# Kernel tuning notes

Hardware: AMD Instinct MI355X
Metric: run time of the kernel (lower is better)

The kernel has to match this reference:

```python
import jax, jax.numpy as jnp
import numpy as np

N, IN_C, OUT_C, E = 10000, 256, 64, 640000


def setup_inputs() -> dict:
    key = jax.random.key(0)
    ks = jax.random.split(key, 12)
    f32 = jnp.float32
    inp = {
        "x": jax.random.normal(ks[0], (N, N), f32),
        "edge_index": jax.random.randint(ks[1], (2, E), 0, N, jnp.int32),
        # trans: Linear(node_num -> in_channels)
        "Wt": jax.random.normal(ks[2], (N, IN_C), f32) / np.float32(np.sqrt(N)),
        "bt": jnp.zeros((IN_C,), f32),
        # conv1: ChebConv(IN_C -> 2*OUT_C), K=2 -> two weight matrices
        "W0_1": jax.random.normal(ks[3], (IN_C, 2 * OUT_C), f32) / np.float32(np.sqrt(IN_C)),
        "W1_1": jax.random.normal(ks[4], (IN_C, 2 * OUT_C), f32) / np.float32(np.sqrt(IN_C)),
        "b1": jnp.zeros((2 * OUT_C,), f32),
        # conv_mu / conv_logstd: ChebConv(2*OUT_C -> OUT_C), K=2
        "W0_mu": jax.random.normal(ks[5], (2 * OUT_C, OUT_C), f32) / np.float32(np.sqrt(2 * OUT_C)),
        "W1_mu": jax.random.normal(ks[6], (2 * OUT_C, OUT_C), f32) / np.float32(np.sqrt(2 * OUT_C)),
        "b_mu": jnp.zeros((OUT_C,), f32),
        "W0_ls": jax.random.normal(ks[7], (2 * OUT_C, OUT_C), f32) / np.float32(np.sqrt(2 * OUT_C)),
        "W1_ls": jax.random.normal(ks[8], (2 * OUT_C, OUT_C), f32) / np.float32(np.sqrt(2 * OUT_C)),
        "b_ls": jnp.zeros((OUT_C,), f32),
    }
    return inp


def _edge_norm(edge_index, n, dtype):
    """ChebConv K=2, sym norm, lambda_max=2: scaled Laplacian L_hat = -D^{-1/2} A D^{-1/2}.
    Returns per-edge weight w_e = -dinv[src] * dinv[dst]."""
    src, dst = edge_index[0], edge_index[1]
    deg = jax.ops.segment_sum(jnp.ones(src.shape, dtype), src, num_segments=n)
    dinv = jnp.where(deg > 0, jax.lax.rsqrt(jnp.maximum(deg, 1.0)), 0.0)
    return -dinv[src] * dinv[dst]


def _cheb(x, src, dst, w, W0, W1, b):
    # Tx_0 = x ; Tx_1 = L_hat @ x via gather-scale-scatter (K=2 stops here)
    tx1 = jax.ops.segment_sum(w[:, None] * x[src], dst, num_segments=x.shape[0])
    return x @ W0 + tx1 @ W1 + b


def reference(x, edge_index, Wt, bt, W0_1, W1_1, b1,
              W0_mu, W1_mu, b_mu, W0_ls, W1_ls, b_ls):
    n = x.shape[0]
    src, dst = edge_index[0], edge_index[1]
    w = _edge_norm(edge_index, n, x.dtype)  # shared across the three convs
    h = jax.nn.relu(x @ Wt + bt)                              # [N, IN_C]
    h = jax.nn.relu(_cheb(h, src, dst, w, W0_1, W1_1, b1))     # [N, 2*OUT_C]
    mu = _cheb(h, src, dst, w, W0_mu, W1_mu, b_mu)             # [N, OUT_C]
    logstd = _cheb(h, src, dst, w, W0_ls, W1_ls, b_ls)         # [N, OUT_C]
    return (mu, logstd)
```

## Files before the change

### kernel.cpp

```cpp
#include <hip/hip_runtime.h>

typedef unsigned short ushort_t;
typedef __bf16 bf16x8 __attribute__((ext_vector_type(8)));
typedef float f32x4 __attribute__((ext_vector_type(4)));

#define GN 10000
#define GE 640000
#define INC 256
#define HID 128
#define OUTC 64

constexpr size_t OFF_WTT   = 0;
constexpr size_t OFF_P     = 5120000;
constexpr size_t OFF_H     = 46276608;
constexpr size_t OFF_TX1   = 56516608;
constexpr size_t OFF_H2    = 66756608;
constexpr size_t OFF_TX2   = 71876608;
constexpr size_t OFF_DEG   = 76996608;
constexpr size_t OFF_INDEG = 77037568;
constexpr size_t OFF_CUR   = 77078528;
constexpr size_t OFF_RP    = 77119488;
constexpr size_t OFF_DINV  = 77160448;
constexpr size_t OFF_CSRC  = 77201408;
constexpr size_t OFF_CSW   = 79761408;

__device__ __forceinline__ ushort_t f2bf(float f) {
  unsigned int u = __float_as_uint(f);
  u += 0x7fffu + ((u >> 16) & 1u);
  return (ushort_t)(u >> 16);
}

__global__ __launch_bounds__(256) void zero_ints(int* __restrict__ p) {
  p[blockIdx.x * 256 + threadIdx.x] = 0;
}

__global__ __launch_bounds__(256) void transpose_wt(const float* __restrict__ Wt,
                                                    ushort_t* __restrict__ WtT) {
  __shared__ float tile[32][33];
  const int tx = threadIdx.x & 31, ty = threadIdx.x >> 5;
  const int k0 = blockIdx.x * 32, c0 = blockIdx.y * 32;
#pragma unroll
  for (int j = 0; j < 4; ++j) {
    const int k = k0 + ty + j * 8;
    if (k < GN) tile[ty + j * 8][tx] = Wt[(size_t)k * INC + c0 + tx];
  }
  __syncthreads();
#pragma unroll
  for (int j = 0; j < 4; ++j) {
    const int c = c0 + ty + j * 8;
    const int k = k0 + tx;
    if (k < GN) WtT[(size_t)c * GN + k] = f2bf(tile[tx][ty + j * 8]);
  }
}

__global__ __launch_bounds__(256) void count_deg(const int* __restrict__ src,
                                                 const int* __restrict__ dst,
                                                 int* __restrict__ outdeg,
                                                 int* __restrict__ indeg) {
  const int e = blockIdx.x * 256 + threadIdx.x;
  atomicAdd(&outdeg[src[e]], 1);
  atomicAdd(&indeg[dst[e]], 1);
}

__global__ __launch_bounds__(256) void dinv_kernel(const int* __restrict__ outdeg,
                                                   float* __restrict__ dinv) {
  const int i = blockIdx.x * 256 + threadIdx.x;
  if (i < GN) {
    const int d = outdeg[i];
    dinv[i] = (d > 0) ? rsqrtf((float)d) : 0.f;
  }
}

__global__ __launch_bounds__(1024) void scan_kernel(const int* __restrict__ indeg,
                                                    int* __restrict__ row_ptr) {
  __shared__ int sdata[1024];
  const int t = threadIdx.x;
  const int base = t * 10;
  int loc[10];
  int s = 0;
#pragma unroll
  for (int j = 0; j < 10; ++j) {
    const int idx = base + j;
    const int v = (idx < GN) ? indeg[idx] : 0;
    loc[j] = v;
    s += v;
  }
  sdata[t] = s;
  __syncthreads();
  for (int off = 1; off < 1024; off <<= 1) {
    int v = 0;
    if (t >= off) v = sdata[t - off];
    __syncthreads();
    if (t >= off) sdata[t] += v;
    __syncthreads();
  }
  int run = sdata[t] - s;
#pragma unroll
  for (int j = 0; j < 10; ++j) {
    const int idx = base + j;
    if (idx <= GN) row_ptr[idx] = run;
    if (idx < GN) run += loc[j];
  }
}

__global__ __launch_bounds__(256) void fill_csr(const int* __restrict__ src,
                                                const int* __restrict__ dst,
                                                const float* __restrict__ dinv,
                                                const int* __restrict__ row_ptr,
                                                int* __restrict__ cursor,
                                                int* __restrict__ csr_src,
                                                float* __restrict__ csr_w) {
  const int e = blockIdx.x * 256 + threadIdx.x;
  const int s = src[e];
  const int d = dst[e];
  const float w = -dinv[s] * dinv[d];
  const int pos = atomicAdd(&cursor[d], 1);
  const int slot = row_ptr[d] + pos;
  csr_src[slot] = s;
  csr_w[slot] = w;
}

__global__ __launch_bounds__(256) void gemm1_kernel(const float* __restrict__ x,
                                                    const ushort_t* __restrict__ WtT,
                                                    float* __restrict__ P) {
  constexpr int LDK = 72;
  __shared__ __align__(16) ushort_t As[64 * LDK];
  __shared__ __align__(16) ushort_t Bs[256 * LDK];
  const int t = threadIdx.x;
  const int rowbase = blockIdx.x * 64;
  const int ks = blockIdx.y;
  const int kbeg = ks * 2560;
  const int kend = min(kbeg + 2560, GN);
  const int nit = (kend - kbeg + 63) >> 6;
  const int lane = t & 63, wave = t >> 6;
  const int m16 = lane & 15, quad = lane >> 4;

  f32x4 acc[4][4];
#pragma unroll
  for (int i = 0; i < 4; ++i)
#pragma unroll
    for (int j = 0; j < 4; ++j) acc[i][j] = {0.f, 0.f, 0.f, 0.f};

  const int ar = t >> 4;
  const int ak = (t & 15) << 2;
  const int bn = t >> 3;
  const int bk = (t & 7) << 3;

  for (int it = 0; it < nit; ++it) {
    const int k0 = kbeg + (it << 6);
#pragma unroll
    for (int i = 0; i < 4; ++i) {
      const int r = ar + i * 16;
      const int row = rowbase + r;
      const int gk = k0 + ak;
      float4 v = make_float4(0.f, 0.f, 0.f, 0.f);
      if (row < GN && gk < kend) v = *(const float4*)(x + (size_t)row * GN + gk);
      ushort4 o = make_ushort4(f2bf(v.x), f2bf(v.y), f2bf(v.z), f2bf(v.w));
      *reinterpret_cast<ushort4*>(&As[r * LDK + ak]) = o;
    }
#pragma unroll
    for (int i = 0; i < 8; ++i) {
      const int n = bn + i * 32;
      const int gk = k0 + bk;
      uint4 v = make_uint4(0u, 0u, 0u, 0u);
      if (gk < kend) v = *(const uint4*)(WtT + (size_t)n * GN + gk);
      *reinterpret_cast<uint4*>(&Bs[n * LDK + bk]) = v;
    }
    __syncthreads();
#pragma unroll
    for (int hh = 0; hh < 2; ++hh) {
      const int kk = hh * 32 + quad * 8;
      bf16x8 a[4], b[4];
#pragma unroll
      for (int mi = 0; mi < 4; ++mi)
        a[mi] = *reinterpret_cast<const bf16x8*>(&As[(mi * 16 + m16) * LDK + kk]);
#pragma unroll
      for (int ni = 0; ni < 4; ++ni)
        b[ni] = *reinterpret_cast<const bf16x8*>(&Bs[(wave * 64 + ni * 16 + m16) * LDK + kk]);
#pragma unroll
      for (int mi = 0; mi < 4; ++mi)
#pragma unroll
        for (int ni = 0; ni < 4; ++ni)
          acc[mi][ni] = __builtin_amdgcn_mfma_f32_16x16x32_bf16(a[mi], b[ni], acc[mi][ni], 0, 0, 0);
    }
    __syncthreads();
  }
#pragma unroll
  for (int mi = 0; mi < 4; ++mi)
#pragma unroll
    for (int ni = 0; ni < 4; ++ni) {
      const int col = wave * 64 + ni * 16 + m16;
      const int row0 = rowbase + mi * 16 + quad * 4;
      float* p = P + ((size_t)ks * 10048 + row0) * 256 + col;
#pragma unroll
      for (int r = 0; r < 4; ++r) p[(size_t)r * 256] = acc[mi][ni][r];
    }
}

__global__ __launch_bounds__(256) void combine_kernel(const float* __restrict__ P,
                                                      const float* __restrict__ bt,
                                                      float* __restrict__ h) {
  const int tid = blockIdx.x * 256 + threadIdx.x;
  const int i = tid >> 6;
  const int c = (tid & 63) << 2;
  const size_t stride = (size_t)10048 * 256;
  const size_t base = (size_t)i * 256 + c;
  const float4 p0 = *(const float4*)(P + 0 * stride + base);
  const float4 p1 = *(const float4*)(P + 1 * stride + base);
  const float4 p2 = *(const float4*)(P + 2 * stride + base);
  const float4 p3 = *(const float4*)(P + 3 * stride + base);
  const float4 bv = *(const float4*)(bt + c);
  float4 o;
  o.x = fmaxf(p0.x + p1.x + p2.x + p3.x + bv.x, 0.f);
  o.y = fmaxf(p0.y + p1.y + p2.y + p3.y + bv.y, 0.f);
  o.z = fmaxf(p0.z + p1.z + p2.z + p3.z + bv.z, 0.f);
  o.w = fmaxf(p0.w + p1.w + p2.w + p3.w + bv.w, 0.f);
  *(float4*)(h + base) = o;
}

template <int C, int NPB>
__global__ __launch_bounds__(256) void spmm_kernel(const float* __restrict__ h,
                                                   const int* __restrict__ row_ptr,
                                                   const int* __restrict__ csr_src,
                                                   const float* __restrict__ csr_w,
                                                   float* __restrict__ tx) {
  const int d = blockIdx.x * NPB + (int)(threadIdx.x / C);
  const int c = threadIdx.x % C;
  const int beg = row_ptr[d];
  const int end = row_ptr[d + 1];
  float acc = 0.f;
#pragma unroll 4
  for (int j = beg; j < end; ++j) {
    const int s = csr_src[j];
    const float w = csr_w[j];
    acc = fmaf(w, h[(size_t)s * C + c], acc);
  }
  tx[(size_t)d * C + c] = acc;
}

__global__ __launch_bounds__(256) void dense1_kernel(const float* __restrict__ h,
                                                     const float* __restrict__ tx,
                                                     const float* __restrict__ W0,
                                                     const float* __restrict__ W1,
                                                     const float* __restrict__ b,
                                                     float* __restrict__ out) {
  const int t = threadIdx.x;
  const int cq = (t & 31) << 2;
  const int rq = t >> 5;
  const int row0 = blockIdx.x * 32 + rq * 4;
  int rowc[4];
#pragma unroll
  for (int r = 0; r < 4; ++r) rowc[r] = min(row0 + r, GN - 1);
  float acc[4][4] = {};
  for (int k = 0; k < INC; k += 4) {
    const float4 w0 = *(const float4*)(W0 + (size_t)(k + 0) * HID + cq);
    const float4 w1 = *(const float4*)(W0 + (size_t)(k + 1) * HID + cq);
    const float4 w2 = *(const float4*)(W0 + (size_t)(k + 2) * HID + cq);
    const float4 w3 = *(const float4*)(W0 + (size_t)(k + 3) * HID + cq);
#pragma unroll
    for (int r = 0; r < 4; ++r) {
      const float4 hv = *(const float4*)(h + (size_t)rowc[r] * INC + k);
      acc[r][0] += hv.x * w0.x + hv.y * w1.x + hv.z * w2.x + hv.w * w3.x;
      acc[r][1] += hv.x * w0.y + hv.y * w1.y + hv.z * w2.y + hv.w * w3.y;
      acc[r][2] += hv.x * w0.z + hv.y * w1.z + hv.z * w2.z + hv.w * w3.z;
      acc[r][3] += hv.x * w0.w + hv.y * w1.w + hv.z * w2.w + hv.w * w3.w;
    }
  }
  for (int k = 0; k < INC; k += 4) {
    const float4 w0 = *(const float4*)(W1 + (size_t)(k + 0) * HID + cq);
    const float4 w1 = *(const float4*)(W1 + (size_t)(k + 1) * HID + cq);
    const float4 w2 = *(const float4*)(W1 + (size_t)(k + 2) * HID + cq);
    const float4 w3 = *(const float4*)(W1 + (size_t)(k + 3) * HID + cq);
#pragma unroll
    for (int r = 0; r < 4; ++r) {
      const float4 hv = *(const float4*)(tx + (size_t)rowc[r] * INC + k);
      acc[r][0] += hv.x * w0.x + hv.y * w1.x + hv.z * w2.x + hv.w * w3.x;
      acc[r][1] += hv.x * w0.y + hv.y * w1.y + hv.z * w2.y + hv.w * w3.y;
      acc[r][2] += hv.x * w0.z + hv.y * w1.z + hv.z * w2.z + hv.w * w3.z;
      acc[r][3] += hv.x * w0.w + hv.y * w1.w + hv.z * w2.w + hv.w * w3.w;
    }
  }
#pragma unroll
  for (int r = 0; r < 4; ++r) {
    const int row = row0 + r;
    if (row < GN) {
      float4 o;
      o.x = fmaxf(acc[r][0] + b[cq + 0], 0.f);
      o.y = fmaxf(acc[r][1] + b[cq + 1], 0.f);
      o.z = fmaxf(acc[r][2] + b[cq + 2], 0.f);
      o.w = fmaxf(acc[r][3] + b[cq + 3], 0.f);
      *(float4*)(out + (size_t)row * HID + cq) = o;
    }
  }
}

__global__ __launch_bounds__(256) void dense2_kernel(const float* __restrict__ h2,
                                                     const float* __restrict__ tx2,
                                                     const float* __restrict__ W0mu,
                                                     const float* __restrict__ W1mu,
                                                     const float* __restrict__ bmu,
                                                     const float* __restrict__ W0ls,
                                                     const float* __restrict__ W1ls,
                                                     const float* __restrict__ bls,
                                                     float* __restrict__ out) {
  const int t = threadIdx.x;
  const int cq = (t & 31) << 2;
  const int rq = t >> 5;
  const int row0 = blockIdx.x * 32 + rq * 4;
  const bool is_mu = (cq < OUTC);
  const int cc = cq & (OUTC - 1);
  const float* Wa = is_mu ? W0mu : W0ls;
  const float* Wb = is_mu ? W1mu : W1ls;
  const float* bb = is_mu ? bmu : bls;
  float* outp = out + (is_mu ? (size_t)0 : (size_t)GN * OUTC);
  int rowc[4];
#pragma unroll
  for (int r = 0; r < 4; ++r) rowc[r] = min(row0 + r, GN - 1);
  float acc[4][4] = {};
  for (int k = 0; k < HID; k += 4) {
    const float4 w0 = *(const float4*)(Wa + (size_t)(k + 0) * OUTC + cc);
    const float4 w1 = *(const float4*)(Wa + (size_t)(k + 1) * OUTC + cc);
    const float4 w2 = *(const float4*)(Wa + (size_t)(k + 2) * OUTC + cc);
    const float4 w3 = *(const float4*)(Wa + (size_t)(k + 3) * OUTC + cc);
#pragma unroll
    for (int r = 0; r < 4; ++r) {
      const float4 hv = *(const float4*)(h2 + (size_t)rowc[r] * HID + k);
      acc[r][0] += hv.x * w0.x + hv.y * w1.x + hv.z * w2.x + hv.w * w3.x;
      acc[r][1] += hv.x * w0.y + hv.y * w1.y + hv.z * w2.y + hv.w * w3.y;
      acc[r][2] += hv.x * w0.z + hv.y * w1.z + hv.z * w2.z + hv.w * w3.z;
      acc[r][3] += hv.x * w0.w + hv.y * w1.w + hv.z * w2.w + hv.w * w3.w;
    }
  }
  for (int k = 0; k < HID; k += 4) {
    const float4 w0 = *(const float4*)(Wb + (size_t)(k + 0) * OUTC + cc);
    const float4 w1 = *(const float4*)(Wb + (size_t)(k + 1) * OUTC + cc);
    const float4 w2 = *(const float4*)(Wb + (size_t)(k + 2) * OUTC + cc);
    const float4 w3 = *(const float4*)(Wb + (size_t)(k + 3) * OUTC + cc);
#pragma unroll
    for (int r = 0; r < 4; ++r) {
      const float4 hv = *(const float4*)(tx2 + (size_t)rowc[r] * HID + k);
      acc[r][0] += hv.x * w0.x + hv.y * w1.x + hv.z * w2.x + hv.w * w3.x;
      acc[r][1] += hv.x * w0.y + hv.y * w1.y + hv.z * w2.y + hv.w * w3.y;
      acc[r][2] += hv.x * w0.z + hv.y * w1.z + hv.z * w2.z + hv.w * w3.z;
      acc[r][3] += hv.x * w0.w + hv.y * w1.w + hv.z * w2.w + hv.w * w3.w;
    }
  }
#pragma unroll
  for (int r = 0; r < 4; ++r) {
    const int row = row0 + r;
    if (row < GN) {
      float4 o;
      o.x = acc[r][0] + bb[cc + 0];
      o.y = acc[r][1] + bb[cc + 1];
      o.z = acc[r][2] + bb[cc + 2];
      o.w = acc[r][3] + bb[cc + 3];
      *(float4*)(outp + (size_t)row * OUTC + cc) = o;
    }
  }
}

extern "C" void kernel_launch(void* const* d_in, const int* in_sizes, int n_in,
                              void* d_out, int out_size, void* d_ws, size_t ws_size,
                              hipStream_t stream) {
  (void)in_sizes; (void)n_in; (void)out_size; (void)ws_size;
  const float* x    = (const float*)d_in[0];
  const int*   ei   = (const int*)d_in[1];
  const float* Wt   = (const float*)d_in[2];
  const float* bt   = (const float*)d_in[3];
  const float* W0_1 = (const float*)d_in[4];
  const float* W1_1 = (const float*)d_in[5];
  const float* b1   = (const float*)d_in[6];
  const float* W0mu = (const float*)d_in[7];
  const float* W1mu = (const float*)d_in[8];
  const float* bmu  = (const float*)d_in[9];
  const float* W0ls = (const float*)d_in[10];
  const float* W1ls = (const float*)d_in[11];
  const float* bls  = (const float*)d_in[12];
  float* out = (float*)d_out;
  char* ws = (char*)d_ws;

  const int* src = ei;
  const int* dst = ei + GE;

  ushort_t* WtT  = (ushort_t*)(ws + OFF_WTT);
  float* P       = (float*)(ws + OFF_P);
  float* h       = (float*)(ws + OFF_H);
  float* tx1     = (float*)(ws + OFF_TX1);
  float* h2      = (float*)(ws + OFF_H2);
  float* tx2     = (float*)(ws + OFF_TX2);
  int* outdeg    = (int*)(ws + OFF_DEG);
  int* indeg     = (int*)(ws + OFF_INDEG);
  int* cursor    = (int*)(ws + OFF_CUR);
  int* row_ptr   = (int*)(ws + OFF_RP);
  float* dinv    = (float*)(ws + OFF_DINV);
  int* csr_src   = (int*)(ws + OFF_CSRC);
  float* csr_w   = (float*)(ws + OFF_CSW);

  zero_ints<<<120, 256, 0, stream>>>(outdeg);
  transpose_wt<<<dim3(313, 8), 256, 0, stream>>>(Wt, WtT);
  count_deg<<<GE / 256, 256, 0, stream>>>(src, dst, outdeg, indeg);
  dinv_kernel<<<40, 256, 0, stream>>>(outdeg, dinv);
  scan_kernel<<<1, 1024, 0, stream>>>(indeg, row_ptr);
  fill_csr<<<GE / 256, 256, 0, stream>>>(src, dst, dinv, row_ptr, cursor, csr_src, csr_w);
  gemm1_kernel<<<dim3(157, 4), 256, 0, stream>>>(x, WtT, P);
  combine_kernel<<<2500, 256, 0, stream>>>(P, bt, h);
  spmm_kernel<256, 1><<<GN, 256, 0, stream>>>(h, row_ptr, csr_src, csr_w, tx1);
  dense1_kernel<<<313, 256, 0, stream>>>(h, tx1, W0_1, W1_1, b1, h2);
  spmm_kernel<128, 2><<<GN / 2, 256, 0, stream>>>(h2, row_ptr, csr_src, csr_w, tx2);
  dense2_kernel<<<313, 256, 0, stream>>>(h2, tx2, W0mu, W1mu, bmu, W0ls, W1ls, bls, out);
}
```

Baseline: 1.045 ms.

## Reassociate first ChebConv, bf16 SpMM gathers, split-K 8 GEMM with direct B loads

Several changes land together. The first ChebConv now multiplies h by W1 before aggregation (L·(hW1) instead of (L·h)W1), so the sparse gather runs on 128 columns instead of 256. Both SpMMs now gather bf16-packed features, one wave per node, halving gather bytes at some precision cost. The main GEMM uses split-K 8 with register prefetch and double-buffered A in shared memory. B is read straight from global memory instead of being staged in LDS, with WtT padded to a 10048 stride.

```diff
diff --git a/kernel.cpp b/kernel.cpp
--- a/kernel.cpp
+++ b/kernel.cpp
@@ -10,25 +10,33 @@
 #define HID 128
 #define OUTC 64
 
+#define KP 10048
+#define SPLITK 8
+#define KCHUNK 1280
+
 constexpr size_t OFF_WTT   = 0;
-constexpr size_t OFF_P     = 5120000;
-constexpr size_t OFF_H     = 46276608;
-constexpr size_t OFF_TX1   = 56516608;
-constexpr size_t OFF_H2    = 66756608;
-constexpr size_t OFF_TX2   = 71876608;
-constexpr size_t OFF_DEG   = 76996608;
-constexpr size_t OFF_INDEG = 77037568;
-constexpr size_t OFF_CUR   = 77078528;
-constexpr size_t OFF_RP    = 77119488;
-constexpr size_t OFF_DINV  = 77160448;
-constexpr size_t OFF_CSRC  = 77201408;
-constexpr size_t OFF_CSW   = 79761408;
+constexpr size_t OFF_P     = OFF_WTT + (size_t)256 * KP * 2;
+constexpr size_t OFF_H     = OFF_P + (size_t)SPLITK * 10048 * 256 * 4;
+constexpr size_t OFF_G1    = OFF_H + (size_t)GN * INC * 4;
+constexpr size_t OFF_TX1   = OFF_G1 + (size_t)GN * HID * 2;
+constexpr size_t OFF_H2    = OFF_TX1 + (size_t)GN * HID * 4;
+constexpr size_t OFF_H2B   = OFF_H2 + (size_t)GN * HID * 4;
+constexpr size_t OFF_TX2   = OFF_H2B + (size_t)GN * HID * 2;
+constexpr size_t OFF_DEG   = OFF_TX2 + (size_t)GN * HID * 4;
+constexpr size_t OFF_INDEG = OFF_DEG + 40960;
+constexpr size_t OFF_CUR   = OFF_INDEG + 40960;
+constexpr size_t OFF_RP    = OFF_CUR + 40960;
+constexpr size_t OFF_DINV  = OFF_RP + 40960;
+constexpr size_t OFF_CSRC  = OFF_DINV + 40960;
+constexpr size_t OFF_CSW   = OFF_CSRC + (size_t)GE * 4;
 
 __device__ __forceinline__ ushort_t f2bf(float f) {
   unsigned int u = __float_as_uint(f);
   u += 0x7fffu + ((u >> 16) & 1u);
   return (ushort_t)(u >> 16);
 }
+__device__ __forceinline__ float bf_lo(unsigned int p) { return __uint_as_float(p << 16); }
+__device__ __forceinline__ float bf_hi(unsigned int p) { return __uint_as_float(p & 0xffff0000u); }
 
 __global__ __launch_bounds__(256) void zero_ints(int* __restrict__ p) {
   p[blockIdx.x * 256 + threadIdx.x] = 0;
@@ -42,14 +50,14 @@
 #pragma unroll
   for (int j = 0; j < 4; ++j) {
     const int k = k0 + ty + j * 8;
-    if (k < GN) tile[ty + j * 8][tx] = Wt[(size_t)k * INC + c0 + tx];
+    tile[ty + j * 8][tx] = (k < GN) ? Wt[(size_t)k * INC + c0 + tx] : 0.f;
   }
   __syncthreads();
 #pragma unroll
   for (int j = 0; j < 4; ++j) {
     const int c = c0 + ty + j * 8;
     const int k = k0 + tx;
-    if (k < GN) WtT[(size_t)c * GN + k] = f2bf(tile[tx][ty + j * 8]);
+    WtT[(size_t)c * KP + k] = f2bf(tile[tx][ty + j * 8]);
   }
 }
 
@@ -120,76 +128,87 @@
   csr_w[slot] = w;
 }
 
-__global__ __launch_bounds__(256) void gemm1_kernel(const float* __restrict__ x,
-                                                    const ushort_t* __restrict__ WtT,
-                                                    float* __restrict__ P) {
+__global__ __launch_bounds__(256, 3) void gemm1_kernel(const float* __restrict__ x,
+                                                       const ushort_t* __restrict__ WtT,
+                                                       float* __restrict__ P) {
   constexpr int LDK = 72;
-  __shared__ __align__(16) ushort_t As[64 * LDK];
-  __shared__ __align__(16) ushort_t Bs[256 * LDK];
-  const int t = threadIdx.x;
+  __shared__ __align__(16) ushort_t As[2][64 * LDK];
+  const int t = threadIdx.x;
+  const int wave = t >> 6, lane = t & 63;
+  const int m16 = lane & 15, quad = lane >> 4;
   const int rowbase = blockIdx.x * 64;
   const int ks = blockIdx.y;
-  const int kbeg = ks * 2560;
-  const int kend = min(kbeg + 2560, GN);
+  const int kbeg = ks * KCHUNK;
+  const int kend = min(kbeg + KCHUNK, GN);
   const int nit = (kend - kbeg + 63) >> 6;
-  const int lane = t & 63, wave = t >> 6;
-  const int m16 = lane & 15, quad = lane >> 4;
-
-  f32x4 acc[4][4];
-#pragma unroll
-  for (int i = 0; i < 4; ++i)
-#pragma unroll
-    for (int j = 0; j < 4; ++j) acc[i][j] = {0.f, 0.f, 0.f, 0.f};
+  const int col0 = wave * 64;
 
   const int ar = t >> 4;
   const int ak = (t & 15) << 2;
-  const int bn = t >> 3;
-  const int bk = (t & 7) << 3;
-
+
+  f32x4 acc[4][4];
+#pragma unroll
+  for (int i = 0; i < 4; ++i)
+#pragma unroll
+    for (int j = 0; j < 4; ++j) acc[i][j] = {0.f, 0.f, 0.f, 0.f};
+
+  float4 va[4];
+  {
+    const int gk = kbeg + ak;
+#pragma unroll
+    for (int i = 0; i < 4; ++i) {
+      const int row = rowbase + ar + i * 16;
+      float4 r = make_float4(0.f, 0.f, 0.f, 0.f);
+      if (row < GN && gk < kend) r = *(const float4*)(x + (size_t)row * GN + gk);
+      va[i] = r;
+    }
+  }
+
+#pragma unroll 2
   for (int it = 0; it < nit; ++it) {
+    ushort_t* Ab = &As[it & 1][0];
+#pragma unroll
+    for (int i = 0; i < 4; ++i) {
+      ushort4 o = make_ushort4(f2bf(va[i].x), f2bf(va[i].y), f2bf(va[i].z), f2bf(va[i].w));
+      *reinterpret_cast<ushort4*>(&Ab[(ar + i * 16) * LDK + ak]) = o;
+    }
+    float4 vb[4] = {};
+    if (it + 1 < nit) {
+      const int gk = kbeg + ((it + 1) << 6) + ak;
+#pragma unroll
+      for (int i = 0; i < 4; ++i) {
+        const int row = rowbase + ar + i * 16;
+        float4 r = make_float4(0.f, 0.f, 0.f, 0.f);
+        if (row < GN && gk < kend) r = *(const float4*)(x + (size_t)row * GN + gk);
+        vb[i] = r;
+      }
+    }
+    __syncthreads();
     const int k0 = kbeg + (it << 6);
-#pragma unroll
-    for (int i = 0; i < 4; ++i) {
-      const int r = ar + i * 16;
-      const int row = rowbase + r;
-      const int gk = k0 + ak;
-      float4 v = make_float4(0.f, 0.f, 0.f, 0.f);
-      if (row < GN && gk < kend) v = *(const float4*)(x + (size_t)row * GN + gk);
-      ushort4 o = make_ushort4(f2bf(v.x), f2bf(v.y), f2bf(v.z), f2bf(v.w));
-      *reinterpret_cast<ushort4*>(&As[r * LDK + ak]) = o;
-    }
-#pragma unroll
-    for (int i = 0; i < 8; ++i) {
-      const int n = bn + i * 32;
-      const int gk = k0 + bk;
-      uint4 v = make_uint4(0u, 0u, 0u, 0u);
-      if (gk < kend) v = *(const uint4*)(WtT + (size_t)n * GN + gk);
-      *reinterpret_cast<uint4*>(&Bs[n * LDK + bk]) = v;
-    }
-    __syncthreads();
 #pragma unroll
     for (int hh = 0; hh < 2; ++hh) {
       const int kk = hh * 32 + quad * 8;
       bf16x8 a[4], b[4];
 #pragma unroll
+      for (int ni = 0; ni < 4; ++ni)
+        b[ni] = *reinterpret_cast<const bf16x8*>(WtT + (size_t)(col0 + ni * 16 + m16) * KP + k0 + kk);
+#pragma unroll
       for (int mi = 0; mi < 4; ++mi)
-        a[mi] = *reinterpret_cast<const bf16x8*>(&As[(mi * 16 + m16) * LDK + kk]);
-#pragma unroll
-      for (int ni = 0; ni < 4; ++ni)
-        b[ni] = *reinterpret_cast<const bf16x8*>(&Bs[(wave * 64 + ni * 16 + m16) * LDK + kk]);
+        a[mi] = *reinterpret_cast<const bf16x8*>(&Ab[(mi * 16 + m16) * LDK + kk]);
 #pragma unroll
       for (int mi = 0; mi < 4; ++mi)
 #pragma unroll
         for (int ni = 0; ni < 4; ++ni)
           acc[mi][ni] = __builtin_amdgcn_mfma_f32_16x16x32_bf16(a[mi], b[ni], acc[mi][ni], 0, 0, 0);
     }
-    __syncthreads();
+#pragma unroll
+    for (int i = 0; i < 4; ++i) va[i] = vb[i];
   }
 #pragma unroll
   for (int mi = 0; mi < 4; ++mi)
 #pragma unroll
     for (int ni = 0; ni < 4; ++ni) {
-      const int col = wave * 64 + ni * 16 + m16;
+      const int col = col0 + ni * 16 + m16;
       const int row0 = rowbase + mi * 16 + quad * 4;
       float* p = P + ((size_t)ks * 10048 + row0) * 256 + col;
 #pragma unroll
@@ -205,45 +224,97 @@
   const int c = (tid & 63) << 2;
   const size_t stride = (size_t)10048 * 256;
   const size_t base = (size_t)i * 256 + c;
-  const float4 p0 = *(const float4*)(P + 0 * stride + base);
-  const float4 p1 = *(const float4*)(P + 1 * stride + base);
-  const float4 p2 = *(const float4*)(P + 2 * stride + base);
-  const float4 p3 = *(const float4*)(P + 3 * stride + base);
+  float4 s = *(const float4*)(P + base);
+#pragma unroll
+  for (int k = 1; k < SPLITK; ++k) {
+    const float4 p = *(const float4*)(P + (size_t)k * stride + base);
+    s.x += p.x; s.y += p.y; s.z += p.z; s.w += p.w;
+  }
   const float4 bv = *(const float4*)(bt + c);
   float4 o;
-  o.x = fmaxf(p0.x + p1.x + p2.x + p3.x + bv.x, 0.f);
-  o.y = fmaxf(p0.y + p1.y + p2.y + p3.y + bv.y, 0.f);
-  o.z = fmaxf(p0.z + p1.z + p2.z + p3.z + bv.z, 0.f);
-  o.w = fmaxf(p0.w + p1.w + p2.w + p3.w + bv.w, 0.f);
+  o.x = fmaxf(s.x + bv.x, 0.f);
+  o.y = fmaxf(s.y + bv.y, 0.f);
+  o.z = fmaxf(s.z + bv.z, 0.f);
+  o.w = fmaxf(s.w + bv.w, 0.f);
   *(float4*)(h + base) = o;
 }
 
-template <int C, int NPB>
-__global__ __launch_bounds__(256) void spmm_kernel(const float* __restrict__ h,
-                                                   const int* __restrict__ row_ptr,
-                                                   const int* __restrict__ csr_src,
-                                                   const float* __restrict__ csr_w,
-                                                   float* __restrict__ tx) {
-  const int d = blockIdx.x * NPB + (int)(threadIdx.x / C);
-  const int c = threadIdx.x % C;
-  const int beg = row_ptr[d];
-  const int end = row_ptr[d + 1];
-  float acc = 0.f;
-#pragma unroll 4
-  for (int j = beg; j < end; ++j) {
-    const int s = csr_src[j];
-    const float w = csr_w[j];
-    acc = fmaf(w, h[(size_t)s * C + c], acc);
-  }
-  tx[(size_t)d * C + c] = acc;
+__global__ __launch_bounds__(256) void dense_g1_kernel(const float* __restrict__ h,
+                                                       const float* __restrict__ W1,
+                                                       ushort_t* __restrict__ g1) {
+  const int t = threadIdx.x;
+  const int cq = (t & 31) << 2;
+  const int rq = t >> 5;
+  const int row0 = blockIdx.x * 32 + rq * 4;
+  int rowc[4];
+#pragma unroll
+  for (int r = 0; r < 4; ++r) rowc[r] = min(row0 + r, GN - 1);
+  float acc[4][4] = {};
+  for (int k = 0; k < INC; k += 4) {
+    const float4 w0 = *(const float4*)(W1 + (size_t)(k + 0) * HID + cq);
+    const float4 w1 = *(const float4*)(W1 + (size_t)(k + 1) * HID + cq);
+    const float4 w2 = *(const float4*)(W1 + (size_t)(k + 2) * HID + cq);
+    const float4 w3 = *(const float4*)(W1 + (size_t)(k + 3) * HID + cq);
+#pragma unroll
+    for (int r = 0; r < 4; ++r) {
+      const float4 hv = *(const float4*)(h + (size_t)rowc[r] * INC + k);
+      acc[r][0] += hv.x * w0.x + hv.y * w1.x + hv.z * w2.x + hv.w * w3.x;
+      acc[r][1] += hv.x * w0.y + hv.y * w1.y + hv.z * w2.y + hv.w * w3.y;
+      acc[r][2] += hv.x * w0.z + hv.y * w1.z + hv.z * w2.z + hv.w * w3.z;
+      acc[r][3] += hv.x * w0.w + hv.y * w1.w + hv.z * w2.w + hv.w * w3.w;
+    }
+  }
+#pragma unroll
+  for (int r = 0; r < 4; ++r) {
+    const int row = row0 + r;
+    if (row < GN) {
+      ushort4 o = make_ushort4(f2bf(acc[r][0]), f2bf(acc[r][1]), f2bf(acc[r][2]), f2bf(acc[r][3]));
+      *reinterpret_cast<ushort4*>(g1 + (size_t)row * HID + cq) = o;
+    }
+  }
+}
+
+__global__ __launch_bounds__(256) void spmm_bf16(const unsigned int* __restrict__ g,
+                                                 const int* __restrict__ row_ptr,
+                                                 const int* __restrict__ csr_src,
+                                                 const float* __restrict__ csr_w,
+                                                 float* __restrict__ tx) {
+  const int t = threadIdx.x;
+  const int node = blockIdx.x * 4 + (t >> 6);
+  const int lane = t & 63;
+  const int beg = row_ptr[node];
+  const int end = row_ptr[node + 1];
+  float a0 = 0.f, a1 = 0.f;
+  int j = beg;
+  for (; j + 1 < end; j += 2) {
+    const int s0 = csr_src[j];
+    const int s1 = csr_src[j + 1];
+    const float w0 = csr_w[j];
+    const float w1 = csr_w[j + 1];
+    const unsigned int p0 = g[(size_t)s0 * 64 + lane];
+    const unsigned int p1 = g[(size_t)s1 * 64 + lane];
+    a0 = fmaf(w0, bf_lo(p0), a0);
+    a1 = fmaf(w0, bf_hi(p0), a1);
+    a0 = fmaf(w1, bf_lo(p1), a0);
+    a1 = fmaf(w1, bf_hi(p1), a1);
+  }
+  if (j < end) {
+    const int s0 = csr_src[j];
+    const float w0 = csr_w[j];
+    const unsigned int p0 = g[(size_t)s0 * 64 + lane];
+    a0 = fmaf(w0, bf_lo(p0), a0);
+    a1 = fmaf(w0, bf_hi(p0), a1);
+  }
+  float2 o = make_float2(a0, a1);
+  *(float2*)(tx + (size_t)node * HID + lane * 2) = o;
 }
 
 __global__ __launch_bounds__(256) void dense1_kernel(const float* __restrict__ h,
                                                      const float* __restrict__ tx,
                                                      const float* __restrict__ W0,
-                                                     const float* __restrict__ W1,
                                                      const float* __restrict__ b,
-                                                     float* __restrict__ out) {
+                                                     float* __restrict__ h2,
+                                                     ushort_t* __restrict__ h2b) {
   const int t = threadIdx.x;
   const int cq = (t & 31) << 2;
   const int rq = t >> 5;
@@ -266,30 +337,20 @@
       acc[r][3] += hv.x * w0.w + hv.y * w1.w + hv.z * w2.w + hv.w * w3.w;
     }
   }
-  for (int k = 0; k < INC; k += 4) {
-    const float4 w0 = *(const float4*)(W1 + (size_t)(k + 0) * HID + cq);
-    const float4 w1 = *(const float4*)(W1 + (size_t)(k + 1) * HID + cq);
-    const float4 w2 = *(const float4*)(W1 + (size_t)(k + 2) * HID + cq);
-    const float4 w3 = *(const float4*)(W1 + (size_t)(k + 3) * HID + cq);
-#pragma unroll
-    for (int r = 0; r < 4; ++r) {
-      const float4 hv = *(const float4*)(tx + (size_t)rowc[r] * INC + k);
-      acc[r][0] += hv.x * w0.x + hv.y * w1.x + hv.z * w2.x + hv.w * w3.x;
-      acc[r][1] += hv.x * w0.y + hv.y * w1.y + hv.z * w2.y + hv.w * w3.y;
-      acc[r][2] += hv.x * w0.z + hv.y * w1.z + hv.z * w2.z + hv.w * w3.z;
-      acc[r][3] += hv.x * w0.w + hv.y * w1.w + hv.z * w2.w + hv.w * w3.w;
-    }
-  }
+  const float4 bv = *(const float4*)(b + cq);
 #pragma unroll
   for (int r = 0; r < 4; ++r) {
     const int row = row0 + r;
     if (row < GN) {
+      const float4 tv = *(const float4*)(tx + (size_t)row * HID + cq);
       float4 o;
-      o.x = fmaxf(acc[r][0] + b[cq + 0], 0.f);
-      o.y = fmaxf(acc[r][1] + b[cq + 1], 0.f);
-      o.z = fmaxf(acc[r][2] + b[cq + 2], 0.f);
-      o.w = fmaxf(acc[r][3] + b[cq + 3], 0.f);
-      *(float4*)(out + (size_t)row * HID + cq) = o;
+      o.x = fmaxf(acc[r][0] + tv.x + bv.x, 0.f);
+      o.y = fmaxf(acc[r][1] + tv.y + bv.y, 0.f);
+      o.z = fmaxf(acc[r][2] + tv.z + bv.z, 0.f);
+      o.w = fmaxf(acc[r][3] + tv.w + bv.w, 0.f);
+      *(float4*)(h2 + (size_t)row * HID + cq) = o;
+      ushort4 ob = make_ushort4(f2bf(o.x), f2bf(o.y), f2bf(o.z), f2bf(o.w));
+      *reinterpret_cast<ushort4*>(h2b + (size_t)row * HID + cq) = ob;
     }
   }
 }
@@ -385,8 +446,10 @@
   ushort_t* WtT  = (ushort_t*)(ws + OFF_WTT);
   float* P       = (float*)(ws + OFF_P);
   float* h       = (float*)(ws + OFF_H);
-  float* tx1     = (float*)(ws + OFF_TX1);
+  ushort_t* g1   = (ushort_t*)(ws + OFF_G1);
+  float* tx1w    = (float*)(ws + OFF_TX1);
   float* h2      = (float*)(ws + OFF_H2);
+  ushort_t* h2b  = (ushort_t*)(ws + OFF_H2B);
   float* tx2     = (float*)(ws + OFF_TX2);
   int* outdeg    = (int*)(ws + OFF_DEG);
   int* indeg     = (int*)(ws + OFF_INDEG);
@@ -397,15 +460,16 @@
   float* csr_w   = (float*)(ws + OFF_CSW);
 
   zero_ints<<<120, 256, 0, stream>>>(outdeg);
-  transpose_wt<<<dim3(313, 8), 256, 0, stream>>>(Wt, WtT);
+  transpose_wt<<<dim3(KP / 32, 8), 256, 0, stream>>>(Wt, WtT);
   count_deg<<<GE / 256, 256, 0, stream>>>(src, dst, outdeg, indeg);
   dinv_kernel<<<40, 256, 0, stream>>>(outdeg, dinv);
   scan_kernel<<<1, 1024, 0, stream>>>(indeg, row_ptr);
   fill_csr<<<GE / 256, 256, 0, stream>>>(src, dst, dinv, row_ptr, cursor, csr_src, csr_w);
-  gemm1_kernel<<<dim3(157, 4), 256, 0, stream>>>(x, WtT, P);
+  gemm1_kernel<<<dim3(157, SPLITK), 256, 0, stream>>>(x, WtT, P);
   combine_kernel<<<2500, 256, 0, stream>>>(P, bt, h);
-  spmm_kernel<256, 1><<<GN, 256, 0, stream>>>(h, row_ptr, csr_src, csr_w, tx1);
-  dense1_kernel<<<313, 256, 0, stream>>>(h, tx1, W0_1, W1_1, b1, h2);
-  spmm_kernel<128, 2><<<GN / 2, 256, 0, stream>>>(h2, row_ptr, csr_src, csr_w, tx2);
+  dense_g1_kernel<<<313, 256, 0, stream>>>(h, W1_1, g1);
+  spmm_bf16<<<2500, 256, 0, stream>>>((const unsigned int*)g1, row_ptr, csr_src, csr_w, tx1w);
+  dense1_kernel<<<313, 256, 0, stream>>>(h, tx1w, W0_1, b1, h2, h2b);
+  spmm_bf16<<<2500, 256, 0, stream>>>((const unsigned int*)h2b, row_ptr, csr_src, csr_w, tx2);
   dense2_kernel<<<313, 256, 0, stream>>>(h2, tx2, W0mu, W1mu, bmu, W0ls, W1ls, bls, out);
 }
```

Measured after the change: 959.2 us. 8.2% less time.
